# Performance work log

Measured on AMD Instinct MI355X. Metric: run time of the kernel, lower is better.

The kernel has to match this reference:

```python
import jax, jax.numpy as jnp
import numpy as np

N = 50000
E = 800000
IN_C = 128
HID_C = 64
OUT_C = 64
HEADS = 4
NEG_SLOPE = 0.2


def setup_inputs() -> dict:
    key = jax.random.key(0)
    ks = jax.random.split(key, 12)
    x = jax.random.normal(ks[0], (N, IN_C), dtype=jnp.float32)
    edge_index = jax.random.randint(ks[1], (2, E), 0, N, dtype=jnp.int32)
    s = 0.1
    # layer 1 params (GATConv: shared lin for src/dst, att vectors per head, bias over H*C)
    W1 = jax.random.normal(ks[2], (IN_C, HEADS * HID_C), dtype=jnp.float32) * s
    att_src1 = jax.random.normal(ks[3], (HEADS, HID_C), dtype=jnp.float32) * s
    att_dst1 = jax.random.normal(ks[4], (HEADS, HID_C), dtype=jnp.float32) * s
    b1 = jnp.zeros((HEADS * HID_C,), dtype=jnp.float32)
    # layer 2 params
    W2 = jax.random.normal(ks[5], (HEADS * HID_C, HEADS * OUT_C), dtype=jnp.float32) * s
    att_src2 = jax.random.normal(ks[6], (HEADS, OUT_C), dtype=jnp.float32) * s
    att_dst2 = jax.random.normal(ks[7], (HEADS, OUT_C), dtype=jnp.float32) * s
    b2 = jnp.zeros((HEADS * OUT_C,), dtype=jnp.float32)
    return {"x": x, "edge_index": edge_index,
            "W1": W1, "att_src1": att_src1, "att_dst1": att_dst1, "b1": b1,
            "W2": W2, "att_src2": att_src2, "att_dst2": att_dst2, "b2": b2}


def _segment_softmax(e, dst, n):
    # e: [E, H], softmax over edges sharing the same dst node, per head
    m = jax.ops.segment_max(e, dst, num_segments=n)        # [N, H]
    ex = jnp.exp(e - m[dst])
    z = jax.ops.segment_sum(ex, dst, num_segments=n)       # [N, H]
    return ex / (z[dst] + 1e-16)


def _gat_layer(x, src, dst, W, att_src, att_dst, bias, heads, out_c):
    n = x.shape[0]
    h = (x @ W).reshape(n, heads, out_c)                   # [N, H, C]
    a_s = jnp.einsum('nhc,hc->nh', h, att_src)             # [N, H]
    a_d = jnp.einsum('nhc,hc->nh', h, att_dst)
    e = jax.nn.leaky_relu(a_s[src] + a_d[dst], NEG_SLOPE)  # [E, H]
    alpha = _segment_softmax(e, dst, n)                    # [E, H]
    msg = alpha[:, :, None] * h[src]                       # [E, H, C]
    out = jax.ops.segment_sum(msg, dst, num_segments=n)    # [N, H, C]
    return out.reshape(n, heads * out_c) + bias


def reference(x, edge_index, W1, att_src1, att_dst1, b1, W2, att_src2, att_dst2, b2):
    # PyG GATConv adds self-loops by default
    loops = jnp.arange(N, dtype=edge_index.dtype)
    src = jnp.concatenate([edge_index[0], loops])
    dst = jnp.concatenate([edge_index[1], loops])
    h = jax.nn.elu(_gat_layer(x, src, dst, W1, att_src1, att_dst1, b1, HEADS, HID_C))
    out = jax.nn.elu(_gat_layer(h, src, dst, W2, att_src2, att_dst2, b2, HEADS, OUT_C))
    return out  # [N, HEADS*OUT_C]
```

## Files before the change

### kernel.cpp

```cpp
#include <hip/hip_runtime.h>
#include <hip/hip_fp16.h>
#include <math.h>


#define LEAKY_SLOPE 0.2f

typedef __attribute__((ext_vector_type(8))) short short8v;
typedef __attribute__((ext_vector_type(4))) float float4v;


__global__ void hist_kernel(const int* __restrict__ ei, int* __restrict__ cnt,
                            int E, int Etot) {
    int e = blockIdx.x * blockDim.x + threadIdx.x;
    if (e >= Etot) return;
    int dst = (e < E) ? ei[E + e] : (e - E);
    atomicAdd(&cnt[dst], 1);
}

__global__ __launch_bounds__(1024) void scan_block(const int* __restrict__ cnt,
                                                   int* __restrict__ row_start,
                                                   int* __restrict__ partials,
                                                   int n) {
    __shared__ int wsum[16];
    int tid = threadIdx.x, lane = tid & 63, wid = tid >> 6;
    int gi = blockIdx.x * 1024 + tid;
    int v = (gi < n) ? cnt[gi] : 0;
    int x = v;
#pragma unroll
    for (int off = 1; off < 64; off <<= 1) {
        int y = __shfl_up(x, off, 64);
        if (lane >= off) x += y;
    }
    if (lane == 63) wsum[wid] = x;
    __syncthreads();
    if (wid == 0 && lane < 16) {
        int w = wsum[lane];
#pragma unroll
        for (int off = 1; off < 16; off <<= 1) {
            int y = __shfl_up(w, off, 16);
            if (lane >= off) w += y;
        }
        wsum[lane] = w;
    }
    __syncthreads();
    int excl = x - v + ((wid > 0) ? wsum[wid - 1] : 0);
    if (gi < n) row_start[gi] = excl;
    if (tid == 1023) partials[blockIdx.x] = wsum[15];
}

__global__ void scan_partials(int* __restrict__ partials, int nb) {
    int lane = threadIdx.x;
    int v = (lane < nb) ? partials[lane] : 0;
    int x = v;
#pragma unroll
    for (int off = 1; off < 64; off <<= 1) {
        int y = __shfl_up(x, off, 64);
        if (lane >= off) x += y;
    }
    if (lane < nb) partials[lane] = x - v;
    if (lane == nb - 1) partials[nb] = x;
}

__global__ __launch_bounds__(1024) void scan_add(int* __restrict__ row_start,
                                                 const int* __restrict__ partials,
                                                 int n, int nb) {
    int gi = blockIdx.x * 1024 + threadIdx.x;
    if (gi < n) row_start[gi] += partials[blockIdx.x];
    if (gi == 0) row_start[n] = partials[nb];
}

__global__ void scatter_kernel(const int* __restrict__ ei,
                               const int* __restrict__ row_start,
                               int* __restrict__ fill,
                               int* __restrict__ edge_src, int E, int Etot) {
    int e = blockIdx.x * blockDim.x + threadIdx.x;
    if (e >= Etot) return;
    int src, dst;
    if (e < E) { src = ei[e]; dst = ei[E + e]; }
    else       { src = e - E; dst = e - E; }
    int pos = row_start[dst] + atomicAdd(&fill[dst], 1);
    edge_src[pos] = src;
}

__global__ void fill_rec(const int* __restrict__ edge_src,
                         const __half* __restrict__ a_s_h,
                         uint4* __restrict__ rec, int Etot) {
    int i = blockIdx.x * blockDim.x + threadIdx.x;
    if (i >= Etot) return;
    int s = edge_src[i];
    uint2 as8 = *(const uint2*)&a_s_h[(size_t)s * 4];
    uint4 r = {(unsigned)s, as8.x, as8.y, 0u};
    rec[i] = r;
}


__device__ __forceinline__ short bf16_rne(float f) {
    unsigned u = __float_as_uint(f);
    return (short)((u + 0x7FFFu + ((u >> 16) & 1u)) >> 16);
}

__device__ __forceinline__ void split_bf16(float f, short& hi, short& lo) {
    unsigned u = __float_as_uint(f);
    hi = (short)(u >> 16);
    float fhi = __uint_as_float(u & 0xFFFF0000u);
    float flo = f - fhi;
    lo = (short)(__float_as_uint(flo) >> 16);
}

template <int K, bool ABF16>
__global__ __launch_bounds__(256) void gemm_mfma(
    const void* __restrict__ Ap, const float* __restrict__ B,
    __half* __restrict__ Ch, const float* __restrict__ att_src,
    const float* __restrict__ att_dst, __half* __restrict__ a_s_out,
    float* __restrict__ a_d_out, int M) {
    __shared__ short As_hi[128][40];
    __shared__ short Bs_hi[128][40];
    __shared__ short Bs_lo[128][40];

    const int col0 = (blockIdx.x & 1) * 128;
    const int row0 = (blockIdx.x >> 1) * 128;
    const int tid = threadIdx.x;
    const int lane = tid & 63;
    const int wave = tid >> 6;
    const int wr = wave >> 1, wc = wave & 1;
    const int quad = lane >> 4, lc = lane & 15;

    float4v acc[4][4] = {};

    const int bn = tid & 127;
    const int bkh = (tid >> 7) * 16;

    for (int k0 = 0; k0 < K; k0 += 32) {
        if constexpr (ABF16) {
            const short* Abf = (const short*)Ap;
#pragma unroll
            for (int i = 0; i < 2; i++) {
                int slot = tid + i * 256;
                int r = slot >> 2;
                int ko = (slot & 3) * 8;
                short8v v = {};
                int gr = row0 + r;
                if (gr < M) v = *(const short8v*)&Abf[(size_t)gr * K + k0 + ko];
                short4 lo4 = {v[0], v[1], v[2], v[3]};
                short4 hi4 = {v[4], v[5], v[6], v[7]};
                *(short4*)&As_hi[r][ko] = lo4;
                *(short4*)&As_hi[r][ko + 4] = hi4;
            }
        } else {
            const float* A = (const float*)Ap;
#pragma unroll
            for (int i = 0; i < 4; i++) {
                int slot = tid + i * 256;
                int r = slot >> 3;
                int kq = (slot & 7) * 4;
                float4 v = {0.f, 0.f, 0.f, 0.f};
                int gr = row0 + r;
                if (gr < M) v = *(const float4*)&A[(size_t)gr * K + k0 + kq];
                short4 h4;
                h4.x = bf16_rne(v.x); h4.y = bf16_rne(v.y);
                h4.z = bf16_rne(v.z); h4.w = bf16_rne(v.w);
                *(short4*)&As_hi[r][kq] = h4;
            }
        }
        {
            float f[16];
#pragma unroll
            for (int j = 0; j < 16; j++)
                f[j] = B[(size_t)(k0 + bkh + j) * 256 + col0 + bn];
            short h8[16], l8[16];
#pragma unroll
            for (int j = 0; j < 16; j++) split_bf16(f[j], h8[j], l8[j]);
#pragma unroll
            for (int j = 0; j < 4; j++) {
                *(short4*)&Bs_hi[bn][bkh + j * 4] = *(short4*)&h8[j * 4];
                *(short4*)&Bs_lo[bn][bkh + j * 4] = *(short4*)&l8[j * 4];
            }
        }
        __syncthreads();

        short8v a_hi[4], b_hi[4], b_lo[4];
#pragma unroll
        for (int mt = 0; mt < 4; mt++) {
            int r = wr * 64 + mt * 16 + lc;
            a_hi[mt] = *(const short8v*)&As_hi[r][quad * 8];
        }
#pragma unroll
        for (int nt = 0; nt < 4; nt++) {
            int n = wc * 64 + nt * 16 + lc;
            b_hi[nt] = *(const short8v*)&Bs_hi[n][quad * 8];
            b_lo[nt] = *(const short8v*)&Bs_lo[n][quad * 8];
        }
#pragma unroll
        for (int mt = 0; mt < 4; mt++)
#pragma unroll
            for (int nt = 0; nt < 4; nt++) {
                acc[mt][nt] = __builtin_amdgcn_mfma_f32_16x16x32_bf16(
                    a_hi[mt], b_hi[nt], acc[mt][nt], 0, 0, 0);
                acc[mt][nt] = __builtin_amdgcn_mfma_f32_16x16x32_bf16(
                    a_hi[mt], b_lo[nt], acc[mt][nt], 0, 0, 0);
            }
        __syncthreads();
    }

    const int head = (col0 >> 6) + wc;
    float as_c[4], ad_c[4];
#pragma unroll
    for (int nt = 0; nt < 4; nt++) {
        as_c[nt] = att_src[head * 64 + nt * 16 + lc];
        ad_c[nt] = att_dst[head * 64 + nt * 16 + lc];
    }

#pragma unroll
    for (int mt = 0; mt < 4; mt++) {
#pragma unroll
        for (int r = 0; r < 4; r++) {
            int gr = row0 + wr * 64 + mt * 16 + quad * 4 + r;
            float ps = 0.f, pd = 0.f;
#pragma unroll
            for (int nt = 0; nt < 4; nt++) {
                float c = acc[mt][nt][r];
                ps = fmaf(c, as_c[nt], ps);
                pd = fmaf(c, ad_c[nt], pd);
                if (gr < M)
                    Ch[(size_t)gr * 256 + col0 + wc * 64 + nt * 16 + lc] =
                        __float2half(c);
            }
#pragma unroll
            for (int off = 1; off < 16; off <<= 1) {
                ps += __shfl_xor(ps, off, 64);
                pd += __shfl_xor(pd, off, 64);
            }
            if (lc == 0 && gr < M) {
                a_s_out[gr * 4 + head] = __float2half(ps);
                a_d_out[gr * 4 + head] = pd;
            }
        }
    }
}


template <bool OUT_BF16>
__global__ __launch_bounds__(256) void gat_aggregate(
    const __half* __restrict__ hh, const uint4* __restrict__ rec,
    const float* __restrict__ a_d, const int* __restrict__ row_start,
    const float* __restrict__ bias, void* __restrict__ outp, int n) {
    int wid = (blockIdx.x * blockDim.x + threadIdx.x) >> 6;
    int lane = threadIdx.x & 63;
    int half = lane >> 5, l32 = lane & 31;
    int node = wid * 2 + half;
    bool valid = (node < n);
    int nd = valid ? node : 0;
    int head = l32 >> 3;

    float ad = a_d[nd * 4 + head];
    int beg = row_start[nd];
    int end = valid ? row_start[nd + 1] : beg;

    float l = 0.f;
    float acc[8] = {};

    int em1 = (end > beg) ? (end - 1) : beg;
    uint4 r0 = rec[beg];
    uint4 r1 = rec[min(beg + 1, em1)];
    uint4 r2 = rec[min(beg + 2, em1)];

#define GATH(rr) (*(const uint4*)&hh[(size_t)(rr).x * 256 + l32 * 8])
#define PROC(rr, vv)                                                      \
    {                                                                     \
        unsigned u = (head & 2) ? (rr).z : (rr).y;                        \
        unsigned short us = (head & 1) ? (unsigned short)(u >> 16)        \
                                       : (unsigned short)(u & 0xFFFFu);   \
        float as = __half2float(*(const __half*)&us);                     \
        float e = as + ad;                                                \
        e = (e > 0.f) ? e : LEAKY_SLOPE * e;                              \
        float w = __expf(e);                                              \
        l += w;                                                           \
        const __half2* hp = (const __half2*)&(vv);                        \
        _Pragma("unroll") for (int j = 0; j < 4; j++) {                   \
            float2 f = __half22float2(hp[j]);                             \
            acc[2 * j] = fmaf(w, f.x, acc[2 * j]);                        \
            acc[2 * j + 1] = fmaf(w, f.y, acc[2 * j + 1]);                \
        }                                                                 \
    }

    uint4 h0 = GATH(r0);
    uint4 h1 = GATH(r1);
    uint4 h2;

    int s = beg;
    while (s < end) {
        h2 = GATH(r2);
        PROC(r0, h0);
        r0 = rec[min(s + 3, em1)];
        if (++s >= end) break;
        h0 = GATH(r0);
        PROC(r1, h1);
        r1 = rec[min(s + 3, em1)];
        if (++s >= end) break;
        h1 = GATH(r1);
        PROC(r2, h2);
        r2 = rec[min(s + 3, em1)];
        ++s;
    }
#undef GATH
#undef PROC

    if (valid) {
        float r = 1.f / l;
        float4 b0 = *(const float4*)&bias[l32 * 8];
        float4 b1 = *(const float4*)&bias[l32 * 8 + 4];
        float o[8];
        o[0] = fmaf(acc[0], r, b0.x); o[1] = fmaf(acc[1], r, b0.y);
        o[2] = fmaf(acc[2], r, b0.z); o[3] = fmaf(acc[3], r, b0.w);
        o[4] = fmaf(acc[4], r, b1.x); o[5] = fmaf(acc[5], r, b1.y);
        o[6] = fmaf(acc[6], r, b1.z); o[7] = fmaf(acc[7], r, b1.w);
#pragma unroll
        for (int j = 0; j < 8; j++)
            o[j] = (o[j] > 0.f) ? o[j] : __expf(o[j]) - 1.f;
        if constexpr (OUT_BF16) {
            short ob[8];
#pragma unroll
            for (int j = 0; j < 8; j++) ob[j] = bf16_rne(o[j]);
            short* outb = (short*)outp;
            *(short4*)&outb[(size_t)node * 256 + l32 * 8] = *(short4*)&ob[0];
            *(short4*)&outb[(size_t)node * 256 + l32 * 8 + 4] = *(short4*)&ob[4];
        } else {
            float* outf = (float*)outp;
            *(float4*)&outf[(size_t)node * 256 + l32 * 8] = *(float4*)&o[0];
            *(float4*)&outf[(size_t)node * 256 + l32 * 8 + 4] = *(float4*)&o[4];
        }
    }
}


extern "C" void kernel_launch(void* const* d_in, const int* in_sizes, int n_in,
                              void* d_out, int out_size, void* d_ws, size_t ws_size,
                              hipStream_t stream) {
    const float* x   = (const float*)d_in[0];
    const int*   ei  = (const int*)d_in[1];
    const float* W1  = (const float*)d_in[2];
    const float* as1 = (const float*)d_in[3];
    const float* ad1 = (const float*)d_in[4];
    const float* b1  = (const float*)d_in[5];
    const float* W2  = (const float*)d_in[6];
    const float* as2 = (const float*)d_in[7];
    const float* ad2 = (const float*)d_in[8];
    const float* b2  = (const float*)d_in[9];
    float* out = (float*)d_out;

    const int N = in_sizes[0] / 128;
    const int E = in_sizes[1] / 2;
    const int Etot = E + N;
    const int NB = (N + 1023) / 1024;

    __half* h_half = (__half*)d_ws;
    short*  x1_bf  = (short*)(h_half + (size_t)N * 256);
    uint4*  rec    = (uint4*)(x1_bf + (size_t)N * 256);
    __half* a_s_h  = (__half*)(rec + Etot);
    float*  a_d    = (float*)(a_s_h + (size_t)N * 4);
    int*    cnt    = (int*)(a_d + (size_t)N * 4);
    int*    fill   = cnt + N;
    int*    row_st = fill + N;
    int*    edge_src = row_st + (N + 1);
    int*    partials = edge_src + Etot;

    hipMemsetAsync(cnt, 0, sizeof(int) * 2 * (size_t)N, stream);
    int eblocks = (Etot + 255) / 256;
    hist_kernel<<<eblocks, 256, 0, stream>>>(ei, cnt, E, Etot);
    scan_block<<<NB, 1024, 0, stream>>>(cnt, row_st, partials, N);
    scan_partials<<<1, 64, 0, stream>>>(partials, NB);
    scan_add<<<NB, 1024, 0, stream>>>(row_st, partials, N, NB);
    scatter_kernel<<<eblocks, 256, 0, stream>>>(ei, row_st, fill, edge_src, E, Etot);

    dim3 ggrid(2 * ((N + 127) / 128));
    int ablocks = (N + 7) / 8;

    gemm_mfma<128, false><<<ggrid, 256, 0, stream>>>(x, W1, h_half, as1, ad1,
                                                     a_s_h, a_d, N);
    fill_rec<<<eblocks, 256, 0, stream>>>(edge_src, a_s_h, rec, Etot);
    gat_aggregate<true><<<ablocks, 256, 0, stream>>>(h_half, rec, a_d, row_st,
                                                     b1, x1_bf, N);
    gemm_mfma<256, true><<<ggrid, 256, 0, stream>>>(x1_bf, W2, h_half, as2, ad2,
                                                    a_s_h, a_d, N);
    fill_rec<<<eblocks, 256, 0, stream>>>(edge_src, a_s_h, rec, Etot);
    gat_aggregate<false><<<ablocks, 256, 0, stream>>>(h_half, rec, a_d, row_st,
                                                      b2, out, N);
}
```

Before: 393.9 us.

## Precompute edge weights in fill_rec, presplit B, one node per wave

```diff
diff --git a/kernel.cpp b/kernel.cpp
--- a/kernel.cpp
+++ b/kernel.cpp
@@ -72,24 +72,36 @@
 __global__ void scatter_kernel(const int* __restrict__ ei,
                                const int* __restrict__ row_start,
                                int* __restrict__ fill,
-                               int* __restrict__ edge_src, int E, int Etot) {
+                               int2* __restrict__ edge_sd, int E, int Etot) {
     int e = blockIdx.x * blockDim.x + threadIdx.x;
     if (e >= Etot) return;
     int src, dst;
     if (e < E) { src = ei[e]; dst = ei[E + e]; }
     else       { src = e - E; dst = e - E; }
     int pos = row_start[dst] + atomicAdd(&fill[dst], 1);
-    edge_src[pos] = src;
-}
-
-__global__ void fill_rec(const int* __restrict__ edge_src,
+    edge_sd[pos] = make_int2(src, dst);
+}
+
+__global__ void fill_rec(const int2* __restrict__ edge_sd,
                          const __half* __restrict__ a_s_h,
+                         const float* __restrict__ a_d,
                          uint4* __restrict__ rec, int Etot) {
     int i = blockIdx.x * blockDim.x + threadIdx.x;
     if (i >= Etot) return;
-    int s = edge_src[i];
-    uint2 as8 = *(const uint2*)&a_s_h[(size_t)s * 4];
-    uint4 r = {(unsigned)s, as8.x, as8.y, 0u};
+    int2 sd = edge_sd[i];
+    uint2 as2 = *(const uint2*)&a_s_h[(size_t)sd.x * 4];
+    float4 ad4 = *(const float4*)&a_d[(size_t)sd.y * 4];
+    float2 f01 = __half22float2(*(const __half2*)&as2.x);
+    float2 f23 = __half22float2(*(const __half2*)&as2.y);
+    float e0 = f01.x + ad4.x, e1 = f01.y + ad4.y;
+    float e2 = f23.x + ad4.z, e3 = f23.y + ad4.w;
+    e0 = (e0 > 0.f) ? e0 : LEAKY_SLOPE * e0;
+    e1 = (e1 > 0.f) ? e1 : LEAKY_SLOPE * e1;
+    e2 = (e2 > 0.f) ? e2 : LEAKY_SLOPE * e2;
+    e3 = (e3 > 0.f) ? e3 : LEAKY_SLOPE * e3;
+    __half2 w01 = __floats2half2_rn(__expf(e0), __expf(e1));
+    __half2 w23 = __floats2half2_rn(__expf(e2), __expf(e3));
+    uint4 r = {(unsigned)sd.x, *(unsigned*)&w01, *(unsigned*)&w23, 0u};
     rec[i] = r;
 }
 
@@ -107,12 +119,24 @@
     lo = (short)(__float_as_uint(flo) >> 16);
 }
 
+__global__ void split_B(const float* __restrict__ B, short* __restrict__ Bt_hi,
+                        short* __restrict__ Bt_lo, int K) {
+    int idx = blockIdx.x * 256 + threadIdx.x;
+    if (idx >= K * 256) return;
+    int k = idx >> 8, c = idx & 255;
+    short hi, lo;
+    split_bf16(B[idx], hi, lo);
+    Bt_hi[c * K + k] = hi;
+    Bt_lo[c * K + k] = lo;
+}
+
+
 template <int K, bool ABF16>
 __global__ __launch_bounds__(256) void gemm_mfma(
-    const void* __restrict__ Ap, const float* __restrict__ B,
-    __half* __restrict__ Ch, const float* __restrict__ att_src,
-    const float* __restrict__ att_dst, __half* __restrict__ a_s_out,
-    float* __restrict__ a_d_out, int M) {
+    const void* __restrict__ Ap, const short* __restrict__ Bt_hi,
+    const short* __restrict__ Bt_lo, __half* __restrict__ Ch,
+    const float* __restrict__ att_src, const float* __restrict__ att_dst,
+    __half* __restrict__ a_s_out, float* __restrict__ a_d_out, int M) {
     __shared__ short As_hi[128][40];
     __shared__ short Bs_hi[128][40];
     __shared__ short Bs_lo[128][40];
@@ -127,9 +151,6 @@
 
     float4v acc[4][4] = {};
 
-    const int bn = tid & 127;
-    const int bkh = (tid >> 7) * 16;
-
     for (int k0 = 0; k0 < K; k0 += 32) {
         if constexpr (ABF16) {
             const short* Abf = (const short*)Ap;
@@ -141,10 +162,7 @@
                 short8v v = {};
                 int gr = row0 + r;
                 if (gr < M) v = *(const short8v*)&Abf[(size_t)gr * K + k0 + ko];
-                short4 lo4 = {v[0], v[1], v[2], v[3]};
-                short4 hi4 = {v[4], v[5], v[6], v[7]};
-                *(short4*)&As_hi[r][ko] = lo4;
-                *(short4*)&As_hi[r][ko + 4] = hi4;
+                *(short8v*)&As_hi[r][ko] = v;
             }
         } else {
             const float* A = (const float*)Ap;
@@ -162,19 +180,16 @@
                 *(short4*)&As_hi[r][kq] = h4;
             }
         }
-        {
-            float f[16];
-#pragma unroll
-            for (int j = 0; j < 16; j++)
-                f[j] = B[(size_t)(k0 + bkh + j) * 256 + col0 + bn];
-            short h8[16], l8[16];
-#pragma unroll
-            for (int j = 0; j < 16; j++) split_bf16(f[j], h8[j], l8[j]);
-#pragma unroll
-            for (int j = 0; j < 4; j++) {
-                *(short4*)&Bs_hi[bn][bkh + j * 4] = *(short4*)&h8[j * 4];
-                *(short4*)&Bs_lo[bn][bkh + j * 4] = *(short4*)&l8[j * 4];
-            }
+#pragma unroll
+        for (int i = 0; i < 2; i++) {
+            int slot = tid + i * 256;
+            int r = slot >> 2;
+            int ko = (slot & 3) * 8;
+            size_t gb = (size_t)(col0 + r) * K + k0 + ko;
+            short8v vh = *(const short8v*)&Bt_hi[gb];
+            short8v vl = *(const short8v*)&Bt_lo[gb];
+            *(short8v*)&Bs_hi[r][ko] = vh;
+            *(short8v*)&Bs_lo[r][ko] = vl;
         }
         __syncthreads();
 
@@ -242,93 +257,88 @@
 template <bool OUT_BF16>
 __global__ __launch_bounds__(256) void gat_aggregate(
     const __half* __restrict__ hh, const uint4* __restrict__ rec,
-    const float* __restrict__ a_d, const int* __restrict__ row_start,
-    const float* __restrict__ bias, void* __restrict__ outp, int n) {
-    int wid = (blockIdx.x * blockDim.x + threadIdx.x) >> 6;
+    const int* __restrict__ row_start, const float* __restrict__ bias,
+    void* __restrict__ outp, int n) {
+    int node = (blockIdx.x * blockDim.x + threadIdx.x) >> 6;
+    if (node >= n) return;
     int lane = threadIdx.x & 63;
-    int half = lane >> 5, l32 = lane & 31;
-    int node = wid * 2 + half;
-    bool valid = (node < n);
-    int nd = valid ? node : 0;
-    int head = l32 >> 3;
-
-    float ad = a_d[nd * 4 + head];
-    int beg = row_start[nd];
-    int end = valid ? row_start[nd + 1] : beg;
+    int head = lane >> 4;
+
+    int beg = row_start[node];
+    int end = row_start[node + 1];
+    int em1 = end - 1;
 
     float l = 0.f;
-    float acc[8] = {};
-
-    int em1 = (end > beg) ? (end - 1) : beg;
+    float acc[4] = {};
+
     uint4 r0 = rec[beg];
     uint4 r1 = rec[min(beg + 1, em1)];
     uint4 r2 = rec[min(beg + 2, em1)];
-
-#define GATH(rr) (*(const uint4*)&hh[(size_t)(rr).x * 256 + l32 * 8])
+    uint4 r3 = rec[min(beg + 3, em1)];
+
+#define GATH(rr) (*(const uint2*)&hh[(size_t)(rr).x * 256 + lane * 4])
 #define PROC(rr, vv)                                                      \
     {                                                                     \
         unsigned u = (head & 2) ? (rr).z : (rr).y;                        \
         unsigned short us = (head & 1) ? (unsigned short)(u >> 16)        \
                                        : (unsigned short)(u & 0xFFFFu);   \
-        float as = __half2float(*(const __half*)&us);                     \
-        float e = as + ad;                                                \
-        e = (e > 0.f) ? e : LEAKY_SLOPE * e;                              \
-        float w = __expf(e);                                              \
+        float w = __half2float(*(const __half*)&us);                      \
         l += w;                                                           \
         const __half2* hp = (const __half2*)&(vv);                        \
-        _Pragma("unroll") for (int j = 0; j < 4; j++) {                   \
-            float2 f = __half22float2(hp[j]);                             \
-            acc[2 * j] = fmaf(w, f.x, acc[2 * j]);                        \
-            acc[2 * j + 1] = fmaf(w, f.y, acc[2 * j + 1]);                \
-        }                                                                 \
-    }
-
-    uint4 h0 = GATH(r0);
-    uint4 h1 = GATH(r1);
-    uint4 h2;
+        float2 f0 = __half22float2(hp[0]);                                \
+        float2 f1 = __half22float2(hp[1]);                                \
+        acc[0] = fmaf(w, f0.x, acc[0]);                                   \
+        acc[1] = fmaf(w, f0.y, acc[1]);                                   \
+        acc[2] = fmaf(w, f1.x, acc[2]);                                   \
+        acc[3] = fmaf(w, f1.y, acc[3]);                                   \
+    }
+
+    uint2 h0 = GATH(r0);
+    uint2 h1 = GATH(r1);
+    uint2 h2 = GATH(r2);
+    uint2 h3;
 
     int s = beg;
     while (s < end) {
-        h2 = GATH(r2);
+        h3 = GATH(r3);
         PROC(r0, h0);
-        r0 = rec[min(s + 3, em1)];
+        r0 = rec[min(s + 4, em1)];
         if (++s >= end) break;
         h0 = GATH(r0);
         PROC(r1, h1);
-        r1 = rec[min(s + 3, em1)];
+        r1 = rec[min(s + 4, em1)];
         if (++s >= end) break;
         h1 = GATH(r1);
         PROC(r2, h2);
-        r2 = rec[min(s + 3, em1)];
+        r2 = rec[min(s + 4, em1)];
+        if (++s >= end) break;
+        h2 = GATH(r2);
+        PROC(r3, h3);
+        r3 = rec[min(s + 4, em1)];
         ++s;
     }
 #undef GATH
 #undef PROC
 
-    if (valid) {
-        float r = 1.f / l;
-        float4 b0 = *(const float4*)&bias[l32 * 8];
-        float4 b1 = *(const float4*)&bias[l32 * 8 + 4];
-        float o[8];
-        o[0] = fmaf(acc[0], r, b0.x); o[1] = fmaf(acc[1], r, b0.y);
-        o[2] = fmaf(acc[2], r, b0.z); o[3] = fmaf(acc[3], r, b0.w);
-        o[4] = fmaf(acc[4], r, b1.x); o[5] = fmaf(acc[5], r, b1.y);
-        o[6] = fmaf(acc[6], r, b1.z); o[7] = fmaf(acc[7], r, b1.w);
-#pragma unroll
-        for (int j = 0; j < 8; j++)
-            o[j] = (o[j] > 0.f) ? o[j] : __expf(o[j]) - 1.f;
-        if constexpr (OUT_BF16) {
-            short ob[8];
-#pragma unroll
-            for (int j = 0; j < 8; j++) ob[j] = bf16_rne(o[j]);
-            short* outb = (short*)outp;
-            *(short4*)&outb[(size_t)node * 256 + l32 * 8] = *(short4*)&ob[0];
-            *(short4*)&outb[(size_t)node * 256 + l32 * 8 + 4] = *(short4*)&ob[4];
-        } else {
-            float* outf = (float*)outp;
-            *(float4*)&outf[(size_t)node * 256 + l32 * 8] = *(float4*)&o[0];
-            *(float4*)&outf[(size_t)node * 256 + l32 * 8 + 4] = *(float4*)&o[4];
-        }
+    float rcp = 1.f / l;
+    float4 b = *(const float4*)&bias[lane * 4];
+    float o[4];
+    o[0] = fmaf(acc[0], rcp, b.x);
+    o[1] = fmaf(acc[1], rcp, b.y);
+    o[2] = fmaf(acc[2], rcp, b.z);
+    o[3] = fmaf(acc[3], rcp, b.w);
+#pragma unroll
+    for (int j = 0; j < 4; j++)
+        o[j] = (o[j] > 0.f) ? o[j] : __expf(o[j]) - 1.f;
+    if constexpr (OUT_BF16) {
+        short ob[4];
+#pragma unroll
+        for (int j = 0; j < 4; j++) ob[j] = bf16_rne(o[j]);
+        short* outb = (short*)outp;
+        *(short4*)&outb[(size_t)node * 256 + lane * 4] = *(short4*)&ob[0];
+    } else {
+        float* outf = (float*)outp;
+        *(float4*)&outf[(size_t)node * 256 + lane * 4] = *(float4*)&o[0];
     }
 }
 
@@ -358,11 +368,18 @@
     uint4*  rec    = (uint4*)(x1_bf + (size_t)N * 256);
     __half* a_s_h  = (__half*)(rec + Etot);
     float*  a_d    = (float*)(a_s_h + (size_t)N * 4);
-    int*    cnt    = (int*)(a_d + (size_t)N * 4);
+    short*  Bt1h   = (short*)(a_d + (size_t)N * 4);
+    short*  Bt1l   = Bt1h + 256 * 128;
+    short*  Bt2h   = Bt1l + 256 * 128;
+    short*  Bt2l   = Bt2h + 256 * 256;
+    int*    cnt    = (int*)(Bt2l + 256 * 256);
     int*    fill   = cnt + N;
     int*    row_st = fill + N;
-    int*    edge_src = row_st + (N + 1);
-    int*    partials = edge_src + Etot;
+    int2*   edge_sd = (int2*)(row_st + (N + 2));
+    int*    partials = (int*)(edge_sd + Etot);
+
+    split_B<<<128, 256, 0, stream>>>(W1, Bt1h, Bt1l, 128);
+    split_B<<<256, 256, 0, stream>>>(W2, Bt2h, Bt2l, 256);
 
     hipMemsetAsync(cnt, 0, sizeof(int) * 2 * (size_t)N, stream);
     int eblocks = (Etot + 255) / 256;
@@ -370,19 +387,19 @@
     scan_block<<<NB, 1024, 0, stream>>>(cnt, row_st, partials, N);
     scan_partials<<<1, 64, 0, stream>>>(partials, NB);
     scan_add<<<NB, 1024, 0, stream>>>(row_st, partials, N, NB);
-    scatter_kernel<<<eblocks, 256, 0, stream>>>(ei, row_st, fill, edge_src, E, Etot);
+    scatter_kernel<<<eblocks, 256, 0, stream>>>(ei, row_st, fill, edge_sd, E, Etot);
 
     dim3 ggrid(2 * ((N + 127) / 128));
-    int ablocks = (N + 7) / 8;
-
-    gemm_mfma<128, false><<<ggrid, 256, 0, stream>>>(x, W1, h_half, as1, ad1,
-                                                     a_s_h, a_d, N);
-    fill_rec<<<eblocks, 256, 0, stream>>>(edge_src, a_s_h, rec, Etot);
-    gat_aggregate<true><<<ablocks, 256, 0, stream>>>(h_half, rec, a_d, row_st,
+    int ablocks = (N + 3) / 4;
+
+    gemm_mfma<128, false><<<ggrid, 256, 0, stream>>>(x, Bt1h, Bt1l, h_half,
+                                                     as1, ad1, a_s_h, a_d, N);
+    fill_rec<<<eblocks, 256, 0, stream>>>(edge_sd, a_s_h, a_d, rec, Etot);
+    gat_aggregate<true><<<ablocks, 256, 0, stream>>>(h_half, rec, row_st,
                                                      b1, x1_bf, N);
-    gemm_mfma<256, true><<<ggrid, 256, 0, stream>>>(x1_bf, W2, h_half, as2, ad2,
-                                                    a_s_h, a_d, N);
-    fill_rec<<<eblocks, 256, 0, stream>>>(edge_src, a_s_h, rec, Etot);
-    gat_aggregate<false><<<ablocks, 256, 0, stream>>>(h_half, rec, a_d, row_st,
+    gemm_mfma<256, true><<<ggrid, 256, 0, stream>>>(x1_bf, Bt2h, Bt2l, h_half,
+                                                    as2, ad2, a_s_h, a_d, N);
+    fill_rec<<<eblocks, 256, 0, stream>>>(edge_sd, a_s_h, a_d, rec, Etot);
+    gat_aggregate<false><<<ablocks, 256, 0, stream>>>(h_half, rec, row_st,
                                                       b2, out, N);
 }
```

Measured after the change: 420.6 us. 6.8% more time.
